# Kernel tuning notes

Hardware: AMD Instinct MI355X
Metric: run time of the kernel (lower is better)

The kernel has to match this reference:

```python
import jax, jax.numpy as jnp
import numpy as np

B, S, D, H, E = 4, 4096, 1024, 16, 8
HID = 4 * D


def _ln(x, g, b, eps=1e-5):
    m = x.mean(-1, keepdims=True)
    v = ((x - m) ** 2).mean(-1, keepdims=True)
    return (x - m) / jnp.sqrt(v + eps) * g + b


def setup_inputs() -> dict:
    key = jax.random.key(0)
    ks = jax.random.split(key, 18)
    s = 0.02
    return {
        "x": jax.random.normal(ks[0], (B, S, D), jnp.float32),
        "conv_w": jax.random.normal(ks[1], (D, D, 3), jnp.float32) * s,
        "conv_b": jnp.zeros((D,), jnp.float32),
        "in_proj_w": jax.random.normal(ks[2], (3 * D, D), jnp.float32) * s,
        "in_proj_b": jnp.zeros((3 * D,), jnp.float32),
        "out_proj_w": jax.random.normal(ks[3], (D, D), jnp.float32) * s,
        "out_proj_b": jnp.zeros((D,), jnp.float32),
        "ln1_g": jnp.ones((D,), jnp.float32),
        "ln1_b": jnp.zeros((D,), jnp.float32),
        "gate_w": jax.random.normal(ks[4], (D, E), jnp.float32) * s,
        "gate_b": jnp.zeros((E,), jnp.float32),
        "w1": jax.random.normal(ks[5], (E, D, HID), jnp.float32) * s,
        "b1": jnp.zeros((E, HID), jnp.float32),
        "w2": jax.random.normal(ks[6], (E, HID, D), jnp.float32) * s,
        "b2": jnp.zeros((E, D), jnp.float32),
        "ln2_g": jnp.ones((D,), jnp.float32),
        "ln2_b": jnp.zeros((D,), jnp.float32),
    }


def reference(x, conv_w, conv_b, in_proj_w, in_proj_b, out_proj_w, out_proj_b,
              ln1_g, ln1_b, gate_w, gate_b, w1, b1, w2, b2, ln2_g, ln2_b):
    b, s, d = x.shape
    h = H
    hd = d // h
    e = w1.shape[0]
    # --- Conv1d over seq axis (kernel 3, padding 1) ---
    xc = jnp.transpose(x, (0, 2, 1))  # (B, D, S)
    xc = jax.lax.conv_general_dilated(
        xc, conv_w, (1,), [(1, 1)], dimension_numbers=("NCH", "OIH", "NCH"))
    x = jnp.transpose(xc + conv_b[None, :, None], (0, 2, 1))  # (B, S, D)
    # --- MultiheadAttention. Faithful to original: batch_first=False, so
    # axis 0 (size B) is treated as the sequence axis, axis 1 (size S) as batch.
    qkv = x @ in_proj_w.T + in_proj_b  # (B, S, 3D)
    q, k, v = jnp.split(qkv, 3, axis=-1)
    q = q.reshape(b, s, h, hd)  # l n h d (l = B, n = S)
    k = k.reshape(b, s, h, hd)
    v = v.reshape(b, s, h, hd)
    scale = 1.0 / jnp.sqrt(jnp.asarray(hd, x.dtype))
    scores = jnp.einsum("lnhd,mnhd->nhlm", q, k) * scale
    attn = jax.nn.softmax(scores, axis=-1)
    o = jnp.einsum("nhlm,mnhd->lnhd", attn, v).reshape(b, s, d)
    attn_out = o @ out_proj_w.T + out_proj_b
    x = _ln(x + attn_out, ln1_g, ln1_b)
    # --- MoE: top-2 gated FFN experts (hidden = 4*dim, ReLU) ---
    xf = x.reshape(-1, d)  # (T, D)
    t = xf.shape[0]
    probs = jax.nn.softmax(xf @ gate_w + gate_b, axis=-1)  # (T, E)
    vals, idx = jax.lax.top_k(probs, 2)
    w = vals / vals.sum(-1, keepdims=True)  # renormalized top-2 weights
    wmat = jnp.zeros((t, e), x.dtype).at[jnp.arange(t)[:, None], idx].add(w)
    y = jnp.zeros_like(xf)
    for ei in range(e):  # small fixed expert loop
        hh = jax.nn.relu(xf @ w1[ei] + b1[ei])
        y = y + wmat[:, ei:ei + 1] * (hh @ w2[ei] + b2[ei])
    moe_out = y.reshape(b, s, d)
    return _ln(x + moe_out, ln2_g, ln2_b)
```

## Files before the change

### kernel.cpp

```cpp
#include <hip/hip_runtime.h>

typedef unsigned short u16;
typedef unsigned int u32;
typedef __attribute__((ext_vector_type(8))) short bf16x8;
typedef __attribute__((ext_vector_type(8))) _Float16 f16x8;
typedef __attribute__((ext_vector_type(4))) float f32x4;

constexpr int Bq = 4, Sq = 4096, Dq = 1024, Hq = 16, Eq = 8, HIDq = 4096;
constexpr int Tq = Bq * Sq;
constexpr long TD = (long)Tq * Dq;
constexpr int PADT = 33792;
constexpr int QCN  = 1024;
constexpr int QROWS = 4 * QCN;
constexpr int ECH  = 4096;
constexpr int MAXC = 3;

constexpr long OFF_XC = 262144;
constexpr long OFF_Q  = OFF_XC + TD;
constexpr long OFF_WT = OFF_Q + (long)QROWS * 3 * Dq;
constexpr long H_B    = OFF_Q * 4;
constexpr long W1E_B  = H_B + (long)2 * ECH * HIDq;
constexpr long W2E_B  = W1E_B + (long)2 * Dq * HIDq;

__device__ __forceinline__ u32 bf1(float x) {
  u32 u = __builtin_bit_cast(u32, x);
  return (u + 0x7fffu + ((u >> 16) & 1u)) >> 16;
}
__device__ __forceinline__ u32 bfpk(float lo, float hi) {
  return bf1(lo) | (bf1(hi) << 16);
}

__device__ __forceinline__ u16 f16b(float v) {
  _Float16 h = (_Float16)v;
  return __builtin_bit_cast(u16, h);
}
__device__ __forceinline__ u32 axpk(float v) {
  _Float16 h = (_Float16)v;
  float hf = (float)h;
  u16 l = f16b((v - hf) * 4096.0f);
  return (u32)l | ((u32)__builtin_bit_cast(u16, h) << 16);
}
__device__ __forceinline__ u32 bxpk(float v) {
  _Float16 h = (_Float16)v;
  float hf = (float)h;
  u16 l = f16b((v - hf) * 4096.0f);
  return (u32)__builtin_bit_cast(u16, h) | ((u32)l << 16);
}

#define BM 128
#define BN 128

#define GLL16(SRC, DST)                                                \
  __builtin_amdgcn_global_load_lds(                                    \
      (const __attribute__((address_space(1))) void*)(SRC),            \
      (__attribute__((address_space(3))) void*)(DST), 16, 0, 0)

__device__ __forceinline__ void xcd_swz(int& bx, int& by) {
  const int nbx = (int)gridDim.x;
  const int nwg = nbx * (int)gridDim.y;
  int bid = (int)blockIdx.y * nbx + (int)blockIdx.x;
  bid = (bid & 7) * (nwg >> 3) + (bid >> 3);
  bx = bid % nbx;
  by = bid / nbx;
}

__device__ __forceinline__ f16x8 hi_octet(const u16* p) {
  const uint4 a = *(const uint4*)p;
  const uint4 b = *(const uint4*)(p + 1024);
  uint4 r;
  r.x = __builtin_amdgcn_perm(a.y, a.x, 0x07060302u);
  r.y = __builtin_amdgcn_perm(a.w, a.z, 0x07060302u);
  r.z = __builtin_amdgcn_perm(b.y, b.x, 0x07060302u);
  r.w = __builtin_amdgcn_perm(b.w, b.z, 0x07060302u);
  return __builtin_bit_cast(f16x8, r);
}
__device__ __forceinline__ f16x8 lo_octet(const u16* p) {
  const uint4 a = *(const uint4*)p;
  const uint4 b = *(const uint4*)(p + 1024);
  uint4 r;
  r.x = __builtin_amdgcn_perm(a.y, a.x, 0x05040100u);
  r.y = __builtin_amdgcn_perm(a.w, a.z, 0x05040100u);
  r.z = __builtin_amdgcn_perm(b.y, b.x, 0x05040100u);
  r.w = __builtin_amdgcn_perm(b.w, b.z, 0x05040100u);
  return __builtin_bit_cast(f16x8, r);
}

template <int AMODE, int EPI>
__global__ __launch_bounds__(256, 2) void gemm_h(
    const float* __restrict__ A, const u16* __restrict__ Bx,
    const float* __restrict__ bias, float* __restrict__ C,
    int Ko, int lda, int ldbN, int ldc, int nbase) {
  __shared__ __align__(16) u16 Asx[8 * 128 * 8];
  __shared__ __align__(16) u16 Bsx[2][8 * 128 * 8];

  const int tid = threadIdx.x;
  int sbx, sby;
  xcd_swz(sbx, sby);
  const int m0 = sby * BM;
  const int n0 = sbx * BN;

  const float* arp[2];
  int abat[2], asrow[2];
  #pragma unroll
  for (int i = 0; i < 2; i++) {
    const int f = tid + 256 * i;
    const int m = f >> 2;
    if (AMODE == 0) {
      arp[i] = A + (long)(m0 + m) * lda;
    } else if (AMODE == 1) {
      abat[i] = (m0 + m) >> 12;
      asrow[i] = (m0 + m) & 4095;
    } else {
      const int mm = m0 + m;
      const int l = mm >> 10;
      const int n = nbase + (mm & 1023);
      arp[i] = A + (long)(l * Sq + n) * lda;
    }
  }

  f32x4 acch[4][4], accx[4][4];
  #pragma unroll
  for (int i = 0; i < 4; i++)
    #pragma unroll
    for (int j = 0; j < 4; j++) {
      acch[i][j] = (f32x4)(0.f);
      accx[i][j] = (f32x4)(0.f);
    }

  const int lane = tid & 63;
  const int wave = tid >> 6;
  const int wr = wave >> 1, wc = wave & 1;
  const int q = lane >> 4, l16 = lane & 15;
  const int abase = wr * 64 + l16;
  const int bbase = wc * 64 + l16;

  auto loadA = [&](int k0, float4 v0[2], float4 v1[2]) {
    #pragma unroll
    for (int i = 0; i < 2; i++) {
      const int f = tid + 256 * i;
      const int kc = f & 3;
      const int kk = k0 + kc * 8;
      float4 a0 = make_float4(0.f, 0.f, 0.f, 0.f), a1 = a0;
      if (AMODE == 1) {
        const int tap = kk >> 10, din = kk & 1023;
        const int sin = asrow[i] + tap - 1;
        if (sin >= 0 && sin < Sq) {
          const float* p = A + ((long)(abat[i] * Sq + sin) * Dq + din);
          a0 = *(const float4*)p;
          a1 = *(const float4*)(p + 4);
        }
      } else {
        a0 = *(const float4*)(arp[i] + kk);
        a1 = *(const float4*)(arp[i] + kk + 4);
      }
      v0[i] = a0;
      v1[i] = a1;
    }
  };

  auto issueB = [&](int k0, int buf) {
    const int kq0 = k0 >> 2;
    #pragma unroll
    for (int i = 0; i < 2; i++) {
      const int f = tid + 256 * i;
      const int kcb = f >> 7, n = f & 127;
      const u16* bp = Bx + ((long)(kq0 + 2 * kcb) * ldbN + n0 + n) * 8;
      GLL16(bp, &Bsx[buf][((2 * kcb) * 128 + n) * 8]);
      GLL16(bp + (long)ldbN * 8, &Bsx[buf][((2 * kcb + 1) * 128 + n) * 8]);
    }
  };

  float4 pv0[2], pv1[2];
  loadA(0, pv0, pv1);
  issueB(0, 0);

  int cur = 0;
  for (int k0 = 0; k0 < Ko; k0 += 32) {
    #pragma unroll
    for (int i = 0; i < 2; i++) {
      const int f = tid + 256 * i;
      const int m = f >> 2, kc = f & 3;
      uint4 wa, wb;
      wa.x = axpk(pv0[i].x);
      wa.y = axpk(pv0[i].y);
      wa.z = axpk(pv0[i].z);
      wa.w = axpk(pv0[i].w);
      wb.x = axpk(pv1[i].x);
      wb.y = axpk(pv1[i].y);
      wb.z = axpk(pv1[i].z);
      wb.w = axpk(pv1[i].w);
      *(uint4*)&Asx[((2 * kc) * 128 + m) * 8] = wa;
      *(uint4*)&Asx[((2 * kc + 1) * 128 + m) * 8] = wb;
    }
    __syncthreads();
    const bool more = (k0 + 32 < Ko);
    if (more) {
      loadA(k0 + 32, pv0, pv1);
      issueB(k0 + 32, cur ^ 1);
    }
    {
      const u16* Bc = Bsx[cur];
      f16x8 af[4], bf[4];
      #pragma unroll
      for (int mf = 0; mf < 4; mf++)
        af[mf] = hi_octet(&Asx[((2 * q) * 128 + abase + mf * 16) * 8]);
      #pragma unroll
      for (int nf = 0; nf < 4; nf++)
        bf[nf] = lo_octet(&Bc[((2 * q) * 128 + bbase + nf * 16) * 8]);
      #pragma unroll
      for (int mf = 0; mf < 4; mf++)
        #pragma unroll
        for (int nf = 0; nf < 4; nf++)
          acch[mf][nf] = __builtin_amdgcn_mfma_f32_16x16x32_f16(
              af[mf], bf[nf], acch[mf][nf], 0, 0, 0);
      #pragma unroll
      for (int s = 0; s < 2; s++) {
        #pragma unroll
        for (int mf = 0; mf < 4; mf++)
          af[mf] =
              *(const f16x8*)&Asx[((s * 4 + q) * 128 + abase + mf * 16) * 8];
        #pragma unroll
        for (int nf = 0; nf < 4; nf++)
          bf[nf] =
              *(const f16x8*)&Bc[((s * 4 + q) * 128 + bbase + nf * 16) * 8];
        #pragma unroll
        for (int mf = 0; mf < 4; mf++)
          #pragma unroll
          for (int nf = 0; nf < 4; nf++)
            accx[mf][nf] = __builtin_amdgcn_mfma_f32_16x16x32_f16(
                af[mf], bf[nf], accx[mf][nf], 0, 0, 0);
      }
    }
    __syncthreads();
    cur ^= 1;
  }

  float bcol[4];
  #pragma unroll
  for (int nf = 0; nf < 4; nf++) bcol[nf] = bias[n0 + wc * 64 + nf * 16 + l16];
  #pragma unroll
  for (int mf = 0; mf < 4; mf++) {
    #pragma unroll
    for (int reg = 0; reg < 4; reg++) {
      const int row = wr * 64 + mf * 16 + q * 4 + reg;
      float* crow = C + (long)(m0 + row) * ldc;
      #pragma unroll
      for (int nf = 0; nf < 4; nf++) {
        const int col = n0 + wc * 64 + nf * 16 + l16;
        float v = acch[mf][nf][reg] + accx[mf][nf][reg] * (1.0f / 4096.0f) +
                  bcol[nf];
        if (EPI == 2) v += crow[col];
        crow[col] = v;
      }
    }
  }
}

template <int AMODE, int EPI>
__global__ __launch_bounds__(256) void gemm_b(
    const void* __restrict__ Av, const u16* __restrict__ Bmf,
    const float* __restrict__ bias, void* __restrict__ Cv,
    int K, int lda, int ldbN, int ldc,
    const int* __restrict__ list, const float* __restrict__ wslot,
    const int* __restrict__ offsp, const int* __restrict__ counts,
    float* __restrict__ moe, int eidx, int cbase) {
  __shared__ __align__(16) u16 As[8 * 128 * 8];
  __shared__ __align__(16) u16 Bs[8 * 128 * 8];

  const int tid = threadIdx.x;
  int sbx, sby;
  xcd_swz(sbx, sby);
  const int rel = cbase + sby * BM;
  const int cnt = counts[eidx];
  const int padded = ((cnt + 127) >> 7) << 7;
  if (rel >= padded) return;
  const int count_e = cnt;
  const int lr0 = rel;
  const int r0 = offsp[eidx] + rel;
  const int n0 = sbx * BN;
  const int mrow0 = sby * BM;

  const float* aptr[4];
  const u16* aptr6[4];
  bool aval[4];
  #pragma unroll
  for (int i = 0; i < 4; i++) {
    const int f = tid + 256 * i;
    const int m = f >> 3;
    aval[i] = true;
    if (AMODE == 5) {
      const int lr = lr0 + m;
      aval[i] = (lr < count_e);
      const int tok = aval[i] ? list[r0 + m] : 0;
      aptr[i] = (const float*)Av + (long)tok * lda;
    } else {
      aptr6[i] = (const u16*)Av + (long)(mrow0 + m) * lda;
    }
  }

  f32x4 acc[4][4];
  #pragma unroll
  for (int i = 0; i < 4; i++)
    #pragma unroll
    for (int j = 0; j < 4; j++) acc[i][j] = (f32x4)(0.f);

  const int lane = tid & 63;
  const int wave = tid >> 6;
  const int wr = wave >> 1, wc = wave & 1;
  const int q = lane >> 4, l16 = lane & 15;

  for (int k0 = 0; k0 < K; k0 += 64) {
    #pragma unroll
    for (int i = 0; i < 4; i++) {
      const int f = tid + 256 * i;
      const int m = f >> 3, kc = f & 7;
      const int kk = k0 + kc * 8;
      uint4 w;
      if (AMODE == 6) {
        w = *(const uint4*)(aptr6[i] + kk);
      } else {
        float4 v0 = make_float4(0.f, 0.f, 0.f, 0.f), v1 = v0;
        if (aval[i]) {
          v0 = *(const float4*)(aptr[i] + kk);
          v1 = *(const float4*)(aptr[i] + kk + 4);
        }
        w.x = bfpk(v0.x, v0.y);
        w.y = bfpk(v0.z, v0.w);
        w.z = bfpk(v1.x, v1.y);
        w.w = bfpk(v1.z, v1.w);
      }
      *(uint4*)&As[(kc * 128 + m) * 8] = w;
    }
    const int kc0 = k0 >> 3;
    #pragma unroll
    for (int i = 0; i < 4; i++) {
      const int f = tid + 256 * i;
      const int kcb = f >> 7, n = f & 127;
      const uint4 wb =
          *(const uint4*)(Bmf + ((long)(kc0 + kcb) * ldbN + n0 + n) * 8);
      *(uint4*)&Bs[(kcb * 128 + n) * 8] = wb;
    }
    __syncthreads();
    #pragma unroll
    for (int s = 0; s < 2; s++) {
      bf16x8 af[4], bfr[4];
      #pragma unroll
      for (int mf = 0; mf < 4; mf++)
        af[mf] = *(const bf16x8*)
            &As[((s * 4 + q) * 128 + wr * 64 + mf * 16 + l16) * 8];
      #pragma unroll
      for (int nf = 0; nf < 4; nf++)
        bfr[nf] = *(const bf16x8*)
            &Bs[((s * 4 + q) * 128 + wc * 64 + nf * 16 + l16) * 8];
      #pragma unroll
      for (int mf = 0; mf < 4; mf++)
        #pragma unroll
        for (int nf = 0; nf < 4; nf++)
          acc[mf][nf] = __builtin_amdgcn_mfma_f32_16x16x32_bf16(
              af[mf], bfr[nf], acc[mf][nf], 0, 0, 0);
    }
    __syncthreads();
  }

  float bcol[4];
  #pragma unroll
  for (int nf = 0; nf < 4; nf++) bcol[nf] = bias[n0 + wc * 64 + nf * 16 + l16];
  #pragma unroll
  for (int mf = 0; mf < 4; mf++) {
    #pragma unroll
    for (int reg = 0; reg < 4; reg++) {
      const int row = wr * 64 + mf * 16 + q * 4 + reg;
      if (lr0 + row >= count_e) continue;
      int tok = 0;
      float wgt = 0.f;
      if (EPI == 3) {
        tok = list[r0 + row];
        wgt = wslot[r0 + row];
      }
      #pragma unroll
      for (int nf = 0; nf < 4; nf++) {
        float v = acc[mf][nf][reg] + bcol[nf];
        const int col = n0 + wc * 64 + nf * 16 + l16;
        if (EPI == 3) {
          float* mp = moe + (long)tok * Dq + col;
          *mp = *mp + wgt * v;
        } else {
          v = fmaxf(v, 0.f);
          ((u16*)Cv)[(long)(mrow0 + row) * ldc + col] = (u16)bf1(v);
        }
      }
    }
  }
}

__global__ __launch_bounds__(256) void wsplit_conv(const float* __restrict__ cw,
                                                   u16* __restrict__ dst) {
  const int n = blockIdx.x * 256 + threadIdx.x;
  const int kc = blockIdx.y;
  uint4 w;
  u32* wp = (u32*)&w;
  #pragma unroll
  for (int j = 0; j < 4; j++) {
    const int k = kc * 4 + j;
    const int tap = k >> 10, din = k & 1023;
    wp[j] = bxpk(cw[(long)n * 3072 + din * 3 + tap]);
  }
  *(uint4*)(dst + ((long)kc * 1024 + n) * 8) = w;
}

__global__ __launch_bounds__(256) void wsplit_nk(const float* __restrict__ src,
                                                 u16* __restrict__ dst, int N,
                                                 int K) {
  const int n = blockIdx.x * 256 + threadIdx.x;
  const int kc = blockIdx.y;
  const float4 v = *(const float4*)(src + (long)n * K + kc * 4);
  uint4 w;
  w.x = bxpk(v.x);
  w.y = bxpk(v.y);
  w.z = bxpk(v.z);
  w.w = bxpk(v.w);
  *(uint4*)(dst + ((long)kc * N + n) * 8) = w;
}

__global__ __launch_bounds__(256) void kn2b_k(const float* __restrict__ src,
                                              u16* __restrict__ dst, int N) {
  const int n = blockIdx.x * 256 + threadIdx.x;
  const int kc = blockIdx.y;
  float v[8];
  #pragma unroll
  for (int j = 0; j < 8; j++) v[j] = src[(long)(kc * 8 + j) * N + n];
  uint4 w;
  w.x = bfpk(v[0], v[1]);
  w.y = bfpk(v[2], v[3]);
  w.z = bfpk(v[4], v[5]);
  w.w = bfpk(v[6], v[7]);
  *(uint4*)(dst + ((long)kc * N + n) * 8) = w;
}

__global__ __launch_bounds__(256) void attn_k(const float* __restrict__ qc,
                                              float* __restrict__ o, int nbase) {
  const int wid = blockIdx.x * 4 + (threadIdx.x >> 6);
  const int lane = threadIdx.x & 63;
  const int h = wid & 15;
  const int nl = wid >> 4;
  float q[4], k[4], v[4];
  #pragma unroll
  for (int l = 0; l < 4; l++) {
    const long base = (long)(l * QCN + nl) * 3072 + h * 64 + lane;
    q[l] = qc[base];
    k[l] = qc[base + Dq];
    v[l] = qc[base + 2 * Dq];
  }
  float sc[4][4];
  #pragma unroll
  for (int l = 0; l < 4; l++)
    #pragma unroll
    for (int m = 0; m < 4; m++) sc[l][m] = q[l] * k[m];
  #pragma unroll
  for (int off = 32; off >= 1; off >>= 1)
    #pragma unroll
    for (int l = 0; l < 4; l++)
      #pragma unroll
      for (int m = 0; m < 4; m++) sc[l][m] += __shfl_xor(sc[l][m], off, 64);
  float p[4][4];
  #pragma unroll
  for (int l = 0; l < 4; l++) {
    float s0[4], mx = -1e30f;
    #pragma unroll
    for (int m = 0; m < 4; m++) { s0[m] = sc[l][m] * 0.125f; mx = fmaxf(mx, s0[m]); }
    float sum = 0.f;
    #pragma unroll
    for (int m = 0; m < 4; m++) { p[l][m] = __expf(s0[m] - mx); sum += p[l][m]; }
    const float inv = 1.0f / sum;
    #pragma unroll
    for (int m = 0; m < 4; m++) p[l][m] *= inv;
  }
  #pragma unroll
  for (int l = 0; l < 4; l++) {
    float ov = 0.f;
    #pragma unroll
    for (int m = 0; m < 4; m++) ov = fmaf(p[l][m], v[m], ov);
    o[(long)(l * Sq + nbase + nl) * Dq + h * 64 + lane] = ov;
  }
}

__device__ __forceinline__ float block_sum256(float v, float* sbuf) {
  #pragma unroll
  for (int off = 32; off >= 1; off >>= 1) v += __shfl_xor(v, off, 64);
  const int w = threadIdx.x >> 6;
  __syncthreads();
  if ((threadIdx.x & 63) == 0) sbuf[w] = v;
  __syncthreads();
  return sbuf[0] + sbuf[1] + sbuf[2] + sbuf[3];
}

__device__ __forceinline__ void ln_core(const float xv[4], const float* g,
                                        const float* bb, float* outp, long base,
                                        float* sbuf) {
  const float tot = block_sum256(xv[0] + xv[1] + xv[2] + xv[3], sbuf);
  const float mean = tot * (1.0f / 1024.0f);
  const float d0 = xv[0] - mean, d1 = xv[1] - mean, d2 = xv[2] - mean,
              d3 = xv[3] - mean;
  const float var =
      block_sum256(d0 * d0 + d1 * d1 + d2 * d2 + d3 * d3, sbuf) * (1.0f / 1024.0f);
  const float inv = 1.0f / sqrtf(var + 1e-5f);
  const int c = threadIdx.x * 4;
  const float4 gg = *(const float4*)(g + c);
  const float4 bv = *(const float4*)(bb + c);
  float4 r;
  r.x = d0 * inv * gg.x + bv.x;
  r.y = d1 * inv * gg.y + bv.y;
  r.z = d2 * inv * gg.z + bv.z;
  r.w = d3 * inv * gg.w + bv.w;
  *(float4*)(outp + base) = r;
}

__global__ __launch_bounds__(256) void ln1_k(const float* __restrict__ xc,
                                             const float* __restrict__ g,
                                             const float* __restrict__ bb,
                                             float* __restrict__ outp) {
  __shared__ float sbuf[4];
  const long base = (long)blockIdx.x * Dq + threadIdx.x * 4;
  const float4 a = *(const float4*)(xc + base);
  const float xv[4] = {a.x, a.y, a.z, a.w};
  ln_core(xv, g, bb, outp, base, sbuf);
}

__global__ __launch_bounds__(256) void ln2_k(const float* __restrict__ x1,
                                             const float* __restrict__ moe,
                                             const float* __restrict__ g,
                                             const float* __restrict__ bb,
                                             float* __restrict__ outp) {
  __shared__ float sbuf[4];
  const long base = (long)blockIdx.x * Dq + threadIdx.x * 4;
  const float4 a = *(const float4*)(x1 + base);
  const float4 m = *(const float4*)(moe + base);
  const float xv[4] = {a.x + m.x, a.y + m.y, a.z + m.z, a.w + m.w};
  ln_core(xv, g, bb, outp, base, sbuf);
}

__global__ __launch_bounds__(256) void gate_k(const float* __restrict__ x1,
                                              const float* __restrict__ gw,
                                              const float* __restrict__ gb,
                                              int* __restrict__ e01,
                                              float* __restrict__ w01) {
  const int t = blockIdx.x * 4 + (threadIdx.x >> 6);
  const int lane = threadIdx.x & 63;
  const float* xr = x1 + (long)t * Dq;
  float acc[8];
  #pragma unroll
  for (int e = 0; e < 8; e++) acc[e] = 0.f;
  #pragma unroll
  for (int j = 0; j < 16; j++) {
    const int d = lane + 64 * j;
    const float xv = xr[d];
    const float4 g0 = *(const float4*)(gw + d * 8);
    const float4 g1 = *(const float4*)(gw + d * 8 + 4);
    acc[0] = fmaf(xv, g0.x, acc[0]);
    acc[1] = fmaf(xv, g0.y, acc[1]);
    acc[2] = fmaf(xv, g0.z, acc[2]);
    acc[3] = fmaf(xv, g0.w, acc[3]);
    acc[4] = fmaf(xv, g1.x, acc[4]);
    acc[5] = fmaf(xv, g1.y, acc[5]);
    acc[6] = fmaf(xv, g1.z, acc[6]);
    acc[7] = fmaf(xv, g1.w, acc[7]);
  }
  #pragma unroll
  for (int off = 32; off >= 1; off >>= 1)
    #pragma unroll
    for (int e = 0; e < 8; e++) acc[e] += __shfl_xor(acc[e], off, 64);
  if (lane == 0) {
    float mx = -1e30f;
    #pragma unroll
    for (int e = 0; e < 8; e++) { acc[e] += gb[e]; mx = fmaxf(mx, acc[e]); }
    float Z = 0.f, p[8];
    #pragma unroll
    for (int e = 0; e < 8; e++) { p[e] = __expf(acc[e] - mx); Z += p[e]; }
    const float invZ = 1.0f / Z;
    float b0 = -1.f, b1 = -1.f;
    int i0 = 0, i1 = 0;
    #pragma unroll
    for (int e = 0; e < 8; e++) {
      const float pe = p[e] * invZ;
      if (pe > b0) { b1 = b0; i1 = i0; b0 = pe; i0 = e; }
      else if (pe > b1) { b1 = pe; i1 = e; }
    }
    const float s = b0 + b1;
    e01[2 * t] = i0;
    e01[2 * t + 1] = i1;
    w01[2 * t] = b0 / s;
    w01[2 * t + 1] = b1 / s;
  }
}

__global__ void zero_k(int* p) {
  if (threadIdx.x < 16) p[threadIdx.x] = 0;
}

__global__ __launch_bounds__(256) void zerof_k(float* __restrict__ p) {
  const long i = ((long)blockIdx.x * 256 + threadIdx.x) * 4;
  *(float4*)(p + i) = make_float4(0.f, 0.f, 0.f, 0.f);
}

__global__ __launch_bounds__(256) void count_k(const int* __restrict__ e01,
                                               int* __restrict__ counts) {
  __shared__ int lc[8];
  const int tid = threadIdx.x;
  if (tid < 8) lc[tid] = 0;
  __syncthreads();
  const int t = blockIdx.x * 256 + tid;
  atomicAdd(&lc[e01[2 * t]], 1);
  atomicAdd(&lc[e01[2 * t + 1]], 1);
  __syncthreads();
  if (tid < 8) atomicAdd(&counts[tid], lc[tid]);
}

__global__ void offs_k(const int* __restrict__ counts, int* __restrict__ offsp) {
  if (threadIdx.x == 0) {
    int a = 0;
    for (int e = 0; e < 8; e++) {
      offsp[e] = a;
      a += ((counts[e] + 127) >> 7) << 7;
    }
    offsp[8] = a;
  }
}

__global__ __launch_bounds__(256) void scatter_k(
    const int* __restrict__ e01, const float* __restrict__ w01,
    int* __restrict__ cursor, const int* __restrict__ offsp,
    int* __restrict__ list, float* __restrict__ wslot) {
  __shared__ int lc[8];
  __shared__ int gbase[8];
  const int tid = threadIdx.x;
  if (tid < 8) lc[tid] = 0;
  __syncthreads();
  const int t = blockIdx.x * 256 + tid;
  const int e0 = e01[2 * t], e1 = e01[2 * t + 1];
  const int p0 = atomicAdd(&lc[e0], 1);
  const int p1 = atomicAdd(&lc[e1], 1);
  __syncthreads();
  if (tid < 8) gbase[tid] = atomicAdd(&cursor[tid], lc[tid]);
  __syncthreads();
  const int s0 = offsp[e0] + gbase[e0] + p0;
  const int s1 = offsp[e1] + gbase[e1] + p1;
  list[s0] = t;
  list[s1] = t;
  wslot[s0] = w01[2 * t];
  wslot[s1] = w01[2 * t + 1];
}

extern "C" void kernel_launch(void* const* d_in, const int* in_sizes, int n_in,
                              void* d_out, int out_size, void* d_ws,
                              size_t ws_size, hipStream_t stream) {
  const float* x          = (const float*)d_in[0];
  const float* conv_w     = (const float*)d_in[1];
  const float* conv_b     = (const float*)d_in[2];
  const float* in_proj_w  = (const float*)d_in[3];
  const float* in_proj_b  = (const float*)d_in[4];
  const float* out_proj_w = (const float*)d_in[5];
  const float* out_proj_b = (const float*)d_in[6];
  const float* ln1_g      = (const float*)d_in[7];
  const float* ln1_b      = (const float*)d_in[8];
  const float* gate_w     = (const float*)d_in[9];
  const float* gate_b     = (const float*)d_in[10];
  const float* w1         = (const float*)d_in[11];
  const float* b1         = (const float*)d_in[12];
  const float* w2         = (const float*)d_in[13];
  const float* b2         = (const float*)d_in[14];
  const float* ln2_g      = (const float*)d_in[15];
  const float* ln2_b      = (const float*)d_in[16];

  float* ws = (float*)d_ws;
  char* wsb = (char*)d_ws;
  int* si      = (int*)ws;
  int* counts  = si;
  int* cursor  = si + 8;
  int* offsp   = si + 16;
  int* e01     = si + 32;
  float* w01   = (float*)(si + 32 + 2 * Tq);
  int* list    = si + 32 + 4 * Tq;
  float* wslot = (float*)(list + PADT);

  float* xc   = ws + OFF_XC;
  float* moe  = ws + OFF_XC;
  float* qc   = ws + OFF_Q;
  u16* wtx    = (u16*)(ws + OFF_WT);
  u16* h      = (u16*)(wsb + H_B);
  u16* w1be   = (u16*)(wsb + W1E_B);
  u16* w2be   = (u16*)(wsb + W2E_B);
  float* o    = (float*)d_out;
  float* x1   = (float*)d_out;
  float* out  = (float*)d_out;

  zero_k<<<1, 64, 0, stream>>>(counts);
  wsplit_conv<<<dim3(4, 768), 256, 0, stream>>>(conv_w, wtx);
  gemm_h<1, 0><<<dim3(Dq / BN, Tq / BM), 256, 0, stream>>>(
      x, wtx, conv_b, xc, 3 * Dq, Dq, Dq, Dq, 0);
  wsplit_nk<<<dim3(12, 256), 256, 0, stream>>>(in_proj_w, wtx, 3 * Dq, Dq);
  for (int c = 0; c < Sq / QCN; c++) {
    gemm_h<4, 0><<<dim3(3 * Dq / BN, QROWS / BM), 256, 0, stream>>>(
        xc, wtx, in_proj_b, qc, Dq, Dq, 3 * Dq, 3 * Dq, c * QCN);
    attn_k<<<(QCN * Hq) / 4, 256, 0, stream>>>(qc, o, c * QCN);
  }
  wsplit_nk<<<dim3(4, 256), 256, 0, stream>>>(out_proj_w, wtx, Dq, Dq);
  gemm_h<0, 2><<<dim3(Dq / BN, Tq / BM), 256, 0, stream>>>(
      o, wtx, out_proj_b, xc, Dq, Dq, Dq, Dq, 0);
  ln1_k<<<Tq, 256, 0, stream>>>(xc, ln1_g, ln1_b, x1);
  zerof_k<<<Tq, 256, 0, stream>>>(moe);
  gate_k<<<Tq / 4, 256, 0, stream>>>(x1, gate_w, gate_b, e01, w01);
  count_k<<<Tq / 256, 256, 0, stream>>>(e01, counts);
  offs_k<<<1, 64, 0, stream>>>(counts, offsp);
  scatter_k<<<Tq / 256, 256, 0, stream>>>(e01, w01, cursor, offsp, list, wslot);
  for (int e = 0; e < Eq; e++) {
    kn2b_k<<<dim3(HIDq / 256, Dq / 8), 256, 0, stream>>>(
        w1 + (long)e * Dq * HIDq, w1be, HIDq);
    kn2b_k<<<dim3(Dq / 256, HIDq / 8), 256, 0, stream>>>(
        w2 + (long)e * HIDq * Dq, w2be, Dq);
    for (int c = 0; c < MAXC; c++) {
      gemm_b<5, 1><<<dim3(HIDq / BN, ECH / BM), 256, 0, stream>>>(
          x1, w1be, b1 + (long)e * HIDq, h, Dq, Dq, HIDq, HIDq,
          list, wslot, offsp, counts, nullptr, e, c * ECH);
      gemm_b<6, 3><<<dim3(Dq / BN, ECH / BM), 256, 0, stream>>>(
          h, w2be, b2 + (long)e * Dq, nullptr, HIDq, HIDq, Dq, Dq,
          list, wslot, offsp, counts, moe, e, c * ECH);
    }
  }
  ln2_k<<<Tq, 256, 0, stream>>>(x1, moe, ln2_g, ln2_b, out);
}
```

Before: 3.635 ms.

## Group all experts into chunked grouped GEMMs with fused weight conversion and split-K

Replaces the per-expert loop, which launched weight-conversion kernels and fixed-size GEMM chunks for each expert, with grouped GEMMs over the concatenated padded expert token lists in 9 chunks. Each block looks up its expert from the offsets. The fp32 weights are read and converted to bf16 directly while loading tiles, and the w2 GEMM is split four ways along K with atomic accumulation into the MoE output. This removes separate conversion passes, launch count and idle blocks for small experts. In exchange, weights are converted redundantly in every block, the weight loads are strided, and the atomics add contention.

```diff
diff --git a/kernel.cpp b/kernel.cpp
--- a/kernel.cpp
+++ b/kernel.cpp
@@ -12,15 +12,13 @@
 constexpr int PADT = 33792;
 constexpr int QCN  = 1024;
 constexpr int QROWS = 4 * QCN;
-constexpr int ECH  = 4096;
-constexpr int MAXC = 3;
+constexpr int GCH  = 4096;
+constexpr int NCH  = 9;
 
 constexpr long OFF_XC = 262144;
 constexpr long OFF_Q  = OFF_XC + TD;
 constexpr long OFF_WT = OFF_Q + (long)QROWS * 3 * Dq;
 constexpr long H_B    = OFF_Q * 4;
-constexpr long W1E_B  = H_B + (long)2 * ECH * HIDq;
-constexpr long W2E_B  = W1E_B + (long)2 * Dq * HIDq;
 
 __device__ __forceinline__ u32 bf1(float x) {
   u32 u = __builtin_bit_cast(u32, x);
@@ -256,46 +254,38 @@
   }
 }
 
-template <int AMODE, int EPI>
-__global__ __launch_bounds__(256) void gemm_b(
-    const void* __restrict__ Av, const u16* __restrict__ Bmf,
-    const float* __restrict__ bias, void* __restrict__ Cv,
-    int K, int lda, int ldbN, int ldc,
-    const int* __restrict__ list, const float* __restrict__ wslot,
-    const int* __restrict__ offsp, const int* __restrict__ counts,
-    float* __restrict__ moe, int eidx, int cbase) {
+__global__ __launch_bounds__(256) void gemm_w1(
+    const float* __restrict__ x1, const float* __restrict__ w1,
+    const float* __restrict__ b1, u16* __restrict__ h,
+    const int* __restrict__ list, const int* __restrict__ offsp,
+    const int* __restrict__ counts, int cbase) {
   __shared__ __align__(16) u16 As[8 * 128 * 8];
   __shared__ __align__(16) u16 Bs[8 * 128 * 8];
 
   const int tid = threadIdx.x;
   int sbx, sby;
   xcd_swz(sbx, sby);
-  const int rel = cbase + sby * BM;
-  const int cnt = counts[eidx];
-  const int padded = ((cnt + 127) >> 7) << 7;
-  if (rel >= padded) return;
-  const int count_e = cnt;
-  const int lr0 = rel;
-  const int r0 = offsp[eidx] + rel;
+  const int r0 = cbase + sby * BM;
+  if (r0 >= offsp[8]) return;
+  int e = 0;
+  #pragma unroll
+  for (int t = 0; t < 7; t++)
+    if (r0 >= offsp[t + 1]) e = t + 1;
+  const int ebase = offsp[e];
+  const int ecnt = counts[e];
   const int n0 = sbx * BN;
-  const int mrow0 = sby * BM;
+  const float* Bw = w1 + (long)e * Dq * HIDq;
+  const float* bias = b1 + (long)e * HIDq;
 
   const float* aptr[4];
-  const u16* aptr6[4];
   bool aval[4];
   #pragma unroll
   for (int i = 0; i < 4; i++) {
     const int f = tid + 256 * i;
     const int m = f >> 3;
-    aval[i] = true;
-    if (AMODE == 5) {
-      const int lr = lr0 + m;
-      aval[i] = (lr < count_e);
-      const int tok = aval[i] ? list[r0 + m] : 0;
-      aptr[i] = (const float*)Av + (long)tok * lda;
-    } else {
-      aptr6[i] = (const u16*)Av + (long)(mrow0 + m) * lda;
-    }
+    aval[i] = (r0 + m - ebase) < ecnt;
+    const int tok = aval[i] ? list[r0 + m] : 0;
+    aptr[i] = x1 + (long)tok * Dq;
   }
 
   f32x4 acc[4][4];
@@ -309,36 +299,38 @@
   const int wr = wave >> 1, wc = wave & 1;
   const int q = lane >> 4, l16 = lane & 15;
 
-  for (int k0 = 0; k0 < K; k0 += 64) {
+  for (int k0 = 0; k0 < Dq; k0 += 64) {
     #pragma unroll
     for (int i = 0; i < 4; i++) {
       const int f = tid + 256 * i;
       const int m = f >> 3, kc = f & 7;
       const int kk = k0 + kc * 8;
+      float4 v0 = make_float4(0.f, 0.f, 0.f, 0.f), v1 = v0;
+      if (aval[i]) {
+        v0 = *(const float4*)(aptr[i] + kk);
+        v1 = *(const float4*)(aptr[i] + kk + 4);
+      }
       uint4 w;
-      if (AMODE == 6) {
-        w = *(const uint4*)(aptr6[i] + kk);
-      } else {
-        float4 v0 = make_float4(0.f, 0.f, 0.f, 0.f), v1 = v0;
-        if (aval[i]) {
-          v0 = *(const float4*)(aptr[i] + kk);
-          v1 = *(const float4*)(aptr[i] + kk + 4);
-        }
-        w.x = bfpk(v0.x, v0.y);
-        w.y = bfpk(v0.z, v0.w);
-        w.z = bfpk(v1.x, v1.y);
-        w.w = bfpk(v1.z, v1.w);
-      }
+      w.x = bfpk(v0.x, v0.y);
+      w.y = bfpk(v0.z, v0.w);
+      w.z = bfpk(v1.x, v1.y);
+      w.w = bfpk(v1.z, v1.w);
       *(uint4*)&As[(kc * 128 + m) * 8] = w;
     }
-    const int kc0 = k0 >> 3;
     #pragma unroll
     for (int i = 0; i < 4; i++) {
       const int f = tid + 256 * i;
       const int kcb = f >> 7, n = f & 127;
-      const uint4 wb =
-          *(const uint4*)(Bmf + ((long)(kc0 + kcb) * ldbN + n0 + n) * 8);
-      *(uint4*)&Bs[(kcb * 128 + n) * 8] = wb;
+      const float* bp = Bw + (long)(k0 + kcb * 8) * HIDq + n0 + n;
+      float v[8];
+      #pragma unroll
+      for (int j = 0; j < 8; j++) v[j] = bp[(long)j * HIDq];
+      uint4 w;
+      w.x = bfpk(v[0], v[1]);
+      w.y = bfpk(v[2], v[3]);
+      w.z = bfpk(v[4], v[5]);
+      w.w = bfpk(v[6], v[7]);
+      *(uint4*)&Bs[(kcb * 128 + n) * 8] = w;
     }
     __syncthreads();
     #pragma unroll
@@ -362,6 +354,7 @@
     __syncthreads();
   }
 
+  const int lrow0 = r0 - cbase;
   float bcol[4];
   #pragma unroll
   for (int nf = 0; nf < 4; nf++) bcol[nf] = bias[n0 + wc * 64 + nf * 16 + l16];
@@ -370,24 +363,121 @@
     #pragma unroll
     for (int reg = 0; reg < 4; reg++) {
       const int row = wr * 64 + mf * 16 + q * 4 + reg;
-      if (lr0 + row >= count_e) continue;
-      int tok = 0;
-      float wgt = 0.f;
-      if (EPI == 3) {
-        tok = list[r0 + row];
-        wgt = wslot[r0 + row];
+      if ((r0 + row - ebase) >= ecnt) continue;
+      #pragma unroll
+      for (int nf = 0; nf < 4; nf++) {
+        float v = fmaxf(acc[mf][nf][reg] + bcol[nf], 0.f);
+        const int col = n0 + wc * 64 + nf * 16 + l16;
+        h[(long)(lrow0 + row) * HIDq + col] = (u16)bf1(v);
       }
+    }
+  }
+}
+
+__global__ __launch_bounds__(256) void gemm_w2(
+    const u16* __restrict__ h, const float* __restrict__ w2,
+    const float* __restrict__ b2, float* __restrict__ moe,
+    const int* __restrict__ list, const float* __restrict__ wslot,
+    const int* __restrict__ offsp, const int* __restrict__ counts,
+    int cbase) {
+  __shared__ __align__(16) u16 As[8 * 128 * 8];
+  __shared__ __align__(16) u16 Bs[8 * 128 * 8];
+
+  const int tid = threadIdx.x;
+  int sbx, sby;
+  xcd_swz(sbx, sby);
+  const int kseg = sby >> 5;
+  const int sblk = sby & 31;
+  const int r0 = cbase + sblk * BM;
+  if (r0 >= offsp[8]) return;
+  int e = 0;
+  #pragma unroll
+  for (int t = 0; t < 7; t++)
+    if (r0 >= offsp[t + 1]) e = t + 1;
+  const int ebase = offsp[e];
+  const int ecnt = counts[e];
+  const int n0 = sbx * BN;
+  const int kstart = kseg * 1024;
+  const float* Bw = w2 + (long)e * HIDq * Dq;
+  const int lrow0 = r0 - cbase;
+
+  f32x4 acc[4][4];
+  #pragma unroll
+  for (int i = 0; i < 4; i++)
+    #pragma unroll
+    for (int j = 0; j < 4; j++) acc[i][j] = (f32x4)(0.f);
+
+  const int lane = tid & 63;
+  const int wave = tid >> 6;
+  const int wr = wave >> 1, wc = wave & 1;
+  const int q = lane >> 4, l16 = lane & 15;
+
+  for (int k0 = kstart; k0 < kstart + 1024; k0 += 64) {
+    #pragma unroll
+    for (int i = 0; i < 4; i++) {
+      const int f = tid + 256 * i;
+      const int m = f >> 3, kc = f & 7;
+      const int kk = k0 + kc * 8;
+      const uint4 w =
+          *(const uint4*)(h + (long)(lrow0 + m) * HIDq + kk);
+      *(uint4*)&As[(kc * 128 + m) * 8] = w;
+    }
+    #pragma unroll
+    for (int i = 0; i < 4; i++) {
+      const int f = tid + 256 * i;
+      const int kcb = f >> 7, n = f & 127;
+      const float* bp = Bw + (long)(k0 + kcb * 8) * Dq + n0 + n;
+      float v[8];
+      #pragma unroll
+      for (int j = 0; j < 8; j++) v[j] = bp[(long)j * Dq];
+      uint4 w;
+      w.x = bfpk(v[0], v[1]);
+      w.y = bfpk(v[2], v[3]);
+      w.z = bfpk(v[4], v[5]);
+      w.w = bfpk(v[6], v[7]);
+      *(uint4*)&Bs[(kcb * 128 + n) * 8] = w;
+    }
+    __syncthreads();
+    #pragma unroll
+    for (int s = 0; s < 2; s++) {
+      bf16x8 af[4], bfr[4];
+      #pragma unroll
+      for (int mf = 0; mf < 4; mf++)
+        af[mf] = *(const bf16x8*)
+            &As[((s * 4 + q) * 128 + wr * 64 + mf * 16 + l16) * 8];
+      #pragma unroll
+      for (int nf = 0; nf < 4; nf++)
+        bfr[nf] = *(const bf16x8*)
+            &Bs[((s * 4 + q) * 128 + wc * 64 + nf * 16 + l16) * 8];
+      #pragma unroll
+      for (int mf = 0; mf < 4; mf++)
+        #pragma unroll
+        for (int nf = 0; nf < 4; nf++)
+          acc[mf][nf] = __builtin_amdgcn_mfma_f32_16x16x32_bf16(
+              af[mf], bfr[nf], acc[mf][nf], 0, 0, 0);
+    }
+    __syncthreads();
+  }
+
+  float bcol[4];
+  #pragma unroll
+  for (int nf = 0; nf < 4; nf++)
+    bcol[nf] = (kseg == 0)
+                   ? b2[(long)e * Dq + n0 + wc * 64 + nf * 16 + l16]
+                   : 0.f;
+  #pragma unroll
+  for (int mf = 0; mf < 4; mf++) {
+    #pragma unroll
+    for (int reg = 0; reg < 4; reg++) {
+      const int row = wr * 64 + mf * 16 + q * 4 + reg;
+      if ((r0 + row - ebase) >= ecnt) continue;
+      const int tok = list[r0 + row];
+      const float wgt = wslot[r0 + row];
       #pragma unroll
       for (int nf = 0; nf < 4; nf++) {
-        float v = acc[mf][nf][reg] + bcol[nf];
+        const float v = acc[mf][nf][reg] + bcol[nf];
         const int col = n0 + wc * 64 + nf * 16 + l16;
-        if (EPI == 3) {
-          float* mp = moe + (long)tok * Dq + col;
-          *mp = *mp + wgt * v;
-        } else {
-          v = fmaxf(v, 0.f);
-          ((u16*)Cv)[(long)(mrow0 + row) * ldc + col] = (u16)bf1(v);
-        }
+        atomicAdd(moe + (long)tok * Dq + col, wgt * v);
       }
     }
   }
@@ -419,21 +509,6 @@
   w.y = bxpk(v.y);
   w.z = bxpk(v.z);
   w.w = bxpk(v.w);
-  *(uint4*)(dst + ((long)kc * N + n) * 8) = w;
-}
-
-__global__ __launch_bounds__(256) void kn2b_k(const float* __restrict__ src,
-                                              u16* __restrict__ dst, int N) {
-  const int n = blockIdx.x * 256 + threadIdx.x;
-  const int kc = blockIdx.y;
-  float v[8];
-  #pragma unroll
-  for (int j = 0; j < 8; j++) v[j] = src[(long)(kc * 8 + j) * N + n];
-  uint4 w;
-  w.x = bfpk(v[0], v[1]);
-  w.y = bfpk(v[2], v[3]);
-  w.z = bfpk(v[4], v[5]);
-  w.w = bfpk(v[6], v[7]);
   *(uint4*)(dst + ((long)kc * N + n) * 8) = w;
 }
 
@@ -687,8 +762,6 @@
   float* qc   = ws + OFF_Q;
   u16* wtx    = (u16*)(ws + OFF_WT);
   u16* h      = (u16*)(wsb + H_B);
-  u16* w1be   = (u16*)(wsb + W1E_B);
-  u16* w2be   = (u16*)(wsb + W2E_B);
   float* o    = (float*)d_out;
   float* x1   = (float*)d_out;
   float* out  = (float*)d_out;
@@ -712,19 +785,11 @@
   count_k<<<Tq / 256, 256, 0, stream>>>(e01, counts);
   offs_k<<<1, 64, 0, stream>>>(counts, offsp);
   scatter_k<<<Tq / 256, 256, 0, stream>>>(e01, w01, cursor, offsp, list, wslot);
-  for (int e = 0; e < Eq; e++) {
-    kn2b_k<<<dim3(HIDq / 256, Dq / 8), 256, 0, stream>>>(
-        w1 + (long)e * Dq * HIDq, w1be, HIDq);
-    kn2b_k<<<dim3(Dq / 256, HIDq / 8), 256, 0, stream>>>(
-        w2 + (long)e * HIDq * Dq, w2be, Dq);
-    for (int c = 0; c < MAXC; c++) {
-      gemm_b<5, 1><<<dim3(HIDq / BN, ECH / BM), 256, 0, stream>>>(
-          x1, w1be, b1 + (long)e * HIDq, h, Dq, Dq, HIDq, HIDq,
-          list, wslot, offsp, counts, nullptr, e, c * ECH);
-      gemm_b<6, 3><<<dim3(Dq / BN, ECH / BM), 256, 0, stream>>>(
-          h, w2be, b2 + (long)e * Dq, nullptr, HIDq, HIDq, Dq, Dq,
-          list, wslot, offsp, counts, moe, e, c * ECH);
-    }
+  for (int c = 0; c < NCH; c++) {
+    gemm_w1<<<dim3(HIDq / BN, GCH / BM), 256, 0, stream>>>(
+        x1, w1, b1, h, list, offsp, counts, c * GCH);
+    gemm_w2<<<dim3(Dq / BN, 4 * (GCH / BM)), 256, 0, stream>>>(
+        h, w2, b2, moe, list, wslot, offsp, counts, c * GCH);
   }
   ln2_k<<<Tq, 256, 0, stream>>>(x1, moe, ln2_g, ln2_b, out);
 }
```

Measured after the change: 3.380 ms. 7.0% less time.
